# Performance work log

Hardware: AMD Instinct MI355X
Metric: run time of the kernel (lower is better)

The kernel has to match this reference:

```python
import jax, jax.numpy as jnp
import numpy as np

L_TEACHER, L_STUDENT = 36, 28
B, H, S, D = 1, 16, 1024, 128
TEMPERATURE = 1.0

def _stride_prior_logits(student, teacher):
    # init: logits[i, j] = -|j - i*teacher/student|
    i = np.arange(student)[:, None].astype(np.float32)
    j = np.arange(teacher)[None, :].astype(np.float32)
    return jnp.asarray(-np.abs(j - i * teacher / student), dtype=jnp.float32)

def setup_inputs() -> dict:
    key = jax.random.key(0)
    k1, k2 = jax.random.split(key)
    ks = jax.random.normal(k1, (L_TEACHER, B, H, S, D), dtype=jnp.float32)
    vs = jax.random.normal(k2, (L_TEACHER, B, H, S, D), dtype=jnp.float32)
    logits = _stride_prior_logits(L_STUDENT, L_TEACHER)
    return {"ks": ks, "vs": vs, "attn_logits_k": logits, "attn_logits_v": logits}

def reference(ks, vs, attn_logits_k, attn_logits_v):
    # softmax over teacher-layer dim, then weighted sum across the 36 layers
    attn_k = jax.nn.softmax(attn_logits_k / TEMPERATURE, axis=-1)  # [28, 36]
    attn_v = jax.nn.softmax(attn_logits_v / TEMPERATURE, axis=-1)  # [28, 36]
    ks_pooled = jnp.einsum('lbhsd,ml->mbhsd', ks, attn_k)  # [28, B, H, S, D]
    vs_pooled = jnp.einsum('lbhsd,ml->mbhsd', vs, attn_v)  # [28, B, H, S, D]
    return (ks_pooled, vs_pooled)
```

## Files before the change

kernel.cpp:

```cpp
#include <hip/hip_runtime.h>
#include <cstddef>


constexpr int LT = 36;
constexpr int LS = 28;
constexpr int N2 = 1048576;
constexpr int TILE = 64;
constexpr int TPT = N2 / TILE;
constexpr int NTILES = 2 * TPT;
constexpr int TPB = 256;
constexpr int NBLOCKS = 768;

__global__ __launch_bounds__(TPB) void pool_kernel(
    const float2* __restrict__ ks,
    const float2* __restrict__ vs,
    const float* __restrict__ lgk,
    const float* __restrict__ lgv,
    float2* __restrict__ out)
{
    __shared__ float2 smA[LT][TILE];
    __shared__ float2 smB[LT][TILE];
    __shared__ __align__(16) float wlK[LS][LT];
    __shared__ __align__(16) float wlV[LS][LT];

    const int tid  = threadIdx.x;
    const int wv   = tid >> 6;
    const int lane = tid & 63;

    const size_t lofs = (size_t)(lane >> 5) * N2 + (size_t)((lane & 31) << 1);

    auto stage = [&](float2 (*buf)[TILE], int t) {
        const float2* src = (t >= TPT) ? vs : ks;
        const size_t c0 = (size_t)(t & (TPT - 1)) * TILE;
        for (int i = wv; i < 18; i += 4) {
            const float2* g = src + (size_t)(2 * i) * N2 + c0 + lofs;
            __builtin_amdgcn_global_load_lds(
                (const __attribute__((address_space(1))) void*)g,
                (__attribute__((address_space(3))) void*)&buf[2 * i][0],
                16, 0, 0);
        }
    };

    int t = blockIdx.x;

    stage(smA, t);
    if (wv < 2 && lane < LS) {
        const float* row = (wv == 0 ? lgk : lgv) + lane * LT;
        float (*wl)[LT] = (wv == 0) ? wlK : wlV;
        float mx = -3.4e38f;
        for (int l = 0; l < LT; ++l) mx = fmaxf(mx, row[l]);
        float s = 0.f;
        for (int l = 0; l < LT; ++l) s += expf(row[l] - mx);
        const float inv = 1.0f / s;
        for (int l = 0; l < LT; ++l) wl[lane][l] = expf(row[l] - mx) * inv;
    }
    __syncthreads();

    float2 (*cur)[TILE] = smA;
    float2 (*nxt)[TILE] = smB;
    const int m0 = 7 * wv;

    for (;;) {
        const int tn = t + NBLOCKS;
        const bool more = (tn < NTILES);

        if (more) stage(nxt, tn);

        if (more) asm volatile("s_waitcnt vmcnt(11)" ::: "memory");
        else      asm volatile("s_waitcnt vmcnt(7)"  ::: "memory");
        __builtin_amdgcn_sched_barrier(0);
        asm volatile("s_barrier" ::: "memory");

        const bool isv = (t >= TPT);
        const float (*wl)[LT] = isv ? wlV : wlK;
        const size_t c0 = (size_t)(t & (TPT - 1)) * TILE;
        float2* dstb = out + (isv ? (size_t)LS * N2 : (size_t)0);

        float2 acc[7];
#pragma unroll
        for (int k = 0; k < 7; ++k) acc[k] = make_float2(0.f, 0.f);

#pragma unroll
        for (int lb = 0; lb < LT / 4; ++lb) {
            float2 d[4];
#pragma unroll
            for (int j = 0; j < 4; ++j) d[j] = cur[4 * lb + j][lane];
#pragma unroll
            for (int k = 0; k < 7; ++k) {
                const float4 w = *reinterpret_cast<const float4*>(&wl[m0 + k][4 * lb]);
                acc[k].x = fmaf(w.x, d[0].x, acc[k].x);
                acc[k].y = fmaf(w.x, d[0].y, acc[k].y);
                acc[k].x = fmaf(w.y, d[1].x, acc[k].x);
                acc[k].y = fmaf(w.y, d[1].y, acc[k].y);
                acc[k].x = fmaf(w.z, d[2].x, acc[k].x);
                acc[k].y = fmaf(w.z, d[2].y, acc[k].y);
                acc[k].x = fmaf(w.w, d[3].x, acc[k].x);
                acc[k].y = fmaf(w.w, d[3].y, acc[k].y);
            }
        }

#pragma unroll
        for (int k = 0; k < 7; ++k) {
            dstb[(size_t)(m0 + k) * N2 + c0 + lane] = acc[k];
        }

        if (!more) break;

        asm volatile("s_barrier" ::: "memory");

        t = tn;
        float2 (*tmp)[TILE] = cur; cur = nxt; nxt = tmp;
    }
}

extern "C" void kernel_launch(void* const* d_in, const int* in_sizes, int n_in,
                              void* d_out, int out_size, void* d_ws, size_t ws_size,
                              hipStream_t stream)
{
    const float2* ks  = (const float2*)d_in[0];
    const float2* vs  = (const float2*)d_in[1];
    const float* lgk  = (const float*)d_in[2];
    const float* lgv  = (const float*)d_in[3];
    float2* out = (float2*)d_out;

    dim3 grid(NBLOCKS);
    dim3 block(TPB);
    hipLaunchKernelGGL(pool_kernel, grid, block, 0, stream,
                       ks, vs, lgk, lgv, out);
}
```

Baseline: 231.7 us.

## Precompute softmax weights in separate kernel and load them via scalar loads

Moves the softmax weight computation into a tiny separate kernel that writes weights to workspace in a layout grouped by four teacher layers. The pool kernel then reads weights with wave-uniform s_load_dwordx4 into SGPRs instead of LDS reads, which frees LDS bandwidth and shrinks LDS use. The grid also grows from 768 to 1024 blocks. This adds a second kernel launch and a serializing s_waitcnt lgkmcnt(0) inside each block of four layers, which may stall the FMA stream.

```diff
diff --git a/kernel.cpp b/kernel.cpp
--- a/kernel.cpp
+++ b/kernel.cpp
@@ -9,23 +9,84 @@
 constexpr int TPT = N2 / TILE;
 constexpr int NTILES = 2 * TPT;
 constexpr int TPB = 256;
-constexpr int NBLOCKS = 768;
+constexpr int NBLOCKS = 1024;
+constexpr int W_TENSOR_STRIDE = 9 * LS * 4;
+
+typedef __attribute__((ext_vector_type(4))) float f32x4;
+
+__global__ __launch_bounds__(64) void softmax_kernel(
+    const float* __restrict__ lgk, const float* __restrict__ lgv,
+    float* __restrict__ ws)
+{
+    const int t = threadIdx.x;
+    const int isv = t >> 5;
+    const int m = t & 31;
+    if (m >= LS) return;
+    const float* row = (isv ? lgv : lgk) + m * LT;
+    float mx = -3.4e38f;
+    for (int l = 0; l < LT; ++l) mx = fmaxf(mx, row[l]);
+    float s = 0.f;
+    for (int l = 0; l < LT; ++l) s += expf(row[l] - mx);
+    const float inv = 1.0f / s;
+    float* o = ws + isv * W_TENSOR_STRIDE;
+    for (int l = 0; l < LT; ++l)
+        o[(l >> 2) * (LS * 4) + m * 4 + (l & 3)] = expf(row[l] - mx) * inv;
+}
+
+template<int LB>
+__device__ __forceinline__ void do_lb(const float* wq,
+                                      const float2 (*cur)[TILE],
+                                      int lane, float2* acc)
+{
+    float2 d[4];
+#pragma unroll
+    for (int j = 0; j < 4; ++j) d[j] = cur[4 * LB + j][lane];
+
+    f32x4 w0, w1, w2, w3, w4, w5, w6;
+    asm volatile(
+        "s_load_dwordx4 %0, %[b], %[o0]\n\t"
+        "s_load_dwordx4 %1, %[b], %[o1]\n\t"
+        "s_load_dwordx4 %2, %[b], %[o2]\n\t"
+        "s_load_dwordx4 %3, %[b], %[o3]\n\t"
+        "s_load_dwordx4 %4, %[b], %[o4]\n\t"
+        "s_load_dwordx4 %5, %[b], %[o5]\n\t"
+        "s_load_dwordx4 %6, %[b], %[o6]\n\t"
+        "s_waitcnt lgkmcnt(0)"
+        : "=s"(w0), "=s"(w1), "=s"(w2), "=s"(w3), "=s"(w4), "=s"(w5), "=s"(w6)
+        : [b] "s"(wq),
+          [o0] "i"(LB * 448 + 0),  [o1] "i"(LB * 448 + 16),
+          [o2] "i"(LB * 448 + 32), [o3] "i"(LB * 448 + 48),
+          [o4] "i"(LB * 448 + 64), [o5] "i"(LB * 448 + 80),
+          [o6] "i"(LB * 448 + 96));
+
+    const f32x4 W[7] = {w0, w1, w2, w3, w4, w5, w6};
+#pragma unroll
+    for (int k = 0; k < 7; ++k) {
+        acc[k].x = fmaf(W[k].x, d[0].x, acc[k].x);
+        acc[k].y = fmaf(W[k].x, d[0].y, acc[k].y);
+        acc[k].x = fmaf(W[k].y, d[1].x, acc[k].x);
+        acc[k].y = fmaf(W[k].y, d[1].y, acc[k].y);
+        acc[k].x = fmaf(W[k].z, d[2].x, acc[k].x);
+        acc[k].y = fmaf(W[k].z, d[2].y, acc[k].y);
+        acc[k].x = fmaf(W[k].w, d[3].x, acc[k].x);
+        acc[k].y = fmaf(W[k].w, d[3].y, acc[k].y);
+    }
+}
 
 __global__ __launch_bounds__(TPB) void pool_kernel(
     const float2* __restrict__ ks,
     const float2* __restrict__ vs,
-    const float* __restrict__ lgk,
-    const float* __restrict__ lgv,
+    const float* __restrict__ ws,
     float2* __restrict__ out)
 {
     __shared__ float2 smA[LT][TILE];
     __shared__ float2 smB[LT][TILE];
-    __shared__ __align__(16) float wlK[LS][LT];
-    __shared__ __align__(16) float wlV[LS][LT];
 
     const int tid  = threadIdx.x;
     const int wv   = tid >> 6;
     const int lane = tid & 63;
+    const int wvu  = __builtin_amdgcn_readfirstlane(wv);
+    const int m0   = 7 * wvu;
 
     const size_t lofs = (size_t)(lane >> 5) * N2 + (size_t)((lane & 31) << 1);
 
@@ -42,23 +103,11 @@
     };
 
     int t = blockIdx.x;
-
     stage(smA, t);
-    if (wv < 2 && lane < LS) {
-        const float* row = (wv == 0 ? lgk : lgv) + lane * LT;
-        float (*wl)[LT] = (wv == 0) ? wlK : wlV;
-        float mx = -3.4e38f;
-        for (int l = 0; l < LT; ++l) mx = fmaxf(mx, row[l]);
-        float s = 0.f;
-        for (int l = 0; l < LT; ++l) s += expf(row[l] - mx);
-        const float inv = 1.0f / s;
-        for (int l = 0; l < LT; ++l) wl[lane][l] = expf(row[l] - mx) * inv;
-    }
     __syncthreads();
 
     float2 (*cur)[TILE] = smA;
     float2 (*nxt)[TILE] = smB;
-    const int m0 = 7 * wv;
 
     for (;;) {
         const int tn = t + NBLOCKS;
@@ -72,7 +121,7 @@
         asm volatile("s_barrier" ::: "memory");
 
         const bool isv = (t >= TPT);
-        const float (*wl)[LT] = isv ? wlV : wlK;
+        const float* wq = ws + (isv ? W_TENSOR_STRIDE : 0) + m0 * 4;
         const size_t c0 = (size_t)(t & (TPT - 1)) * TILE;
         float2* dstb = out + (isv ? (size_t)LS * N2 : (size_t)0);
 
@@ -80,24 +129,15 @@
 #pragma unroll
         for (int k = 0; k < 7; ++k) acc[k] = make_float2(0.f, 0.f);
 
-#pragma unroll
-        for (int lb = 0; lb < LT / 4; ++lb) {
-            float2 d[4];
-#pragma unroll
-            for (int j = 0; j < 4; ++j) d[j] = cur[4 * lb + j][lane];
-#pragma unroll
-            for (int k = 0; k < 7; ++k) {
-                const float4 w = *reinterpret_cast<const float4*>(&wl[m0 + k][4 * lb]);
-                acc[k].x = fmaf(w.x, d[0].x, acc[k].x);
-                acc[k].y = fmaf(w.x, d[0].y, acc[k].y);
-                acc[k].x = fmaf(w.y, d[1].x, acc[k].x);
-                acc[k].y = fmaf(w.y, d[1].y, acc[k].y);
-                acc[k].x = fmaf(w.z, d[2].x, acc[k].x);
-                acc[k].y = fmaf(w.z, d[2].y, acc[k].y);
-                acc[k].x = fmaf(w.w, d[3].x, acc[k].x);
-                acc[k].y = fmaf(w.w, d[3].y, acc[k].y);
-            }
-        }
+        do_lb<0>(wq, cur, lane, acc);
+        do_lb<1>(wq, cur, lane, acc);
+        do_lb<2>(wq, cur, lane, acc);
+        do_lb<3>(wq, cur, lane, acc);
+        do_lb<4>(wq, cur, lane, acc);
+        do_lb<5>(wq, cur, lane, acc);
+        do_lb<6>(wq, cur, lane, acc);
+        do_lb<7>(wq, cur, lane, acc);
+        do_lb<8>(wq, cur, lane, acc);
 
 #pragma unroll
         for (int k = 0; k < 7; ++k) {
@@ -121,10 +161,11 @@
     const float2* vs  = (const float2*)d_in[1];
     const float* lgk  = (const float*)d_in[2];
     const float* lgv  = (const float*)d_in[3];
+    float* ws = (float*)d_ws;
     float2* out = (float2*)d_out;
 
-    dim3 grid(NBLOCKS);
-    dim3 block(TPB);
-    hipLaunchKernelGGL(pool_kernel, grid, block, 0, stream,
-                       ks, vs, lgk, lgv, out);
+    hipLaunchKernelGGL(softmax_kernel, dim3(1), dim3(64), 0, stream,
+                       lgk, lgv, ws);
+    hipLaunchKernelGGL(pool_kernel, dim3(NBLOCKS), dim3(TPB), 0, stream,
+                       ks, vs, ws, out);
 }
```

After: 238.4 us. 1.03x slower.
